# Optimization experiments

Hardware: AMD Instinct MI355X
Metric: run time of the kernel (lower is better)

Reference implementation:

```python
import jax, jax.numpy as jnp
import numpy as np

HEADS = 16
LORA_ALPHA = 1.0
LORA_R = 8.0


def setup_inputs() -> dict:
    key = jax.random.key(0)
    ks = jax.random.split(key, 7)
    B, S, D, R = 4, 2048, 1024, 8
    s = 0.02
    return {
        "x": jax.random.normal(ks[0], (B, S, D), dtype=jnp.float32),
        "lora_A": jax.random.normal(ks[1], (R, D), dtype=jnp.float32) * s,
        "lora_B": jax.random.normal(ks[2], (3 * D, R), dtype=jnp.float32) * s,
        "W_qkv": jax.random.normal(ks[3], (3 * D, D), dtype=jnp.float32) * s,
        "b_qkv": jax.random.normal(ks[4], (3 * D,), dtype=jnp.float32) * s,
        "W_proj": jax.random.normal(ks[5], (D, D), dtype=jnp.float32) * s,
        "b_proj": jax.random.normal(ks[6], (D,), dtype=jnp.float32) * s,
    }


def reference(x, lora_A, lora_B, W_qkv, b_qkv, W_proj, b_proj):
    B, S, D = x.shape
    H = HEADS
    Hd = D // H
    scale = Hd ** -0.5

    # qkv projection: x @ W_qkv.T + b  -> [B, S, 3D]
    qkv = jnp.einsum("bsd,ed->bse", x, W_qkv) + b_qkv
    # LoRA branch: (x @ A.T) @ B.T * (alpha / r)
    lora = jnp.einsum("bsr,er->bse", jnp.einsum("bsd,rd->bsr", x, lora_A), lora_B)
    qkv = qkv + lora * (LORA_ALPHA / LORA_R)

    qkv = qkv.reshape(B, S, 3, H, Hd).transpose(2, 0, 3, 1, 4)
    q, k, v = qkv[0], qkv[1], qkv[2]

    attn = jnp.einsum("bhqd,bhkd->bhqk", q, k) * scale
    attn = jax.nn.softmax(attn, axis=-1)  # dropout is identity in eval mode
    out = jnp.einsum("bhqk,bhkd->bhqd", attn, v)
    out = out.transpose(0, 2, 1, 3).reshape(B, S, D)
    out = jnp.einsum("bsd,ed->bse", out, W_proj) + b_proj
    return out
```

## Files before the change

### kernel.cpp

```cpp
#include <hip/hip_runtime.h>
#include <hip/hip_bf16.h>

typedef __bf16 bf16_t;
typedef __bf16 bf16x8 __attribute__((ext_vector_type(8)));
typedef float f32x4 __attribute__((ext_vector_type(4)));

#define MFMA16(a, b, c) __builtin_amdgcn_mfma_f32_16x16x32_bf16((a), (b), (c), 0, 0, 0)

__device__ __forceinline__ void gload16(const bf16_t* g, bf16_t* l) {
  __builtin_amdgcn_global_load_lds((const __attribute__((address_space(1))) void*)g,
                                   (__attribute__((address_space(3))) void*)l,
                                   16, 0, 0);
}

__global__ void __launch_bounds__(256)
prep_kernel(const float* __restrict__ x, const float* __restrict__ lA,
            const float* __restrict__ lB, const float* __restrict__ Wq,
            const float* __restrict__ Wp,
            bf16_t* __restrict__ xh, bf16_t* __restrict__ We,
            bf16_t* __restrict__ Wph) {
  const int bid = blockIdx.x, tid = threadIdx.x;
  if (bid < 4096) {
    const size_t i = ((size_t)bid * 256 + tid) * 8;
    const float4 f0 = ((const float4*)(x + i))[0];
    const float4 f1 = ((const float4*)(x + i))[1];
    alignas(16) bf16_t o[8] = {(bf16_t)f0.x, (bf16_t)f0.y, (bf16_t)f0.z, (bf16_t)f0.w,
                               (bf16_t)f1.x, (bf16_t)f1.y, (bf16_t)f1.z, (bf16_t)f1.w};
    *(uint4*)(xh + i) = *(const uint4*)o;
  } else if (bid < 7168) {
    const int g = (bid - 4096) * 256 + tid;
    const int e = g >> 8;
    const int d4 = (g & 255) * 4;
    float4 a = ((const float4*)(Wq + (size_t)e * 1024 + d4))[0];
#pragma unroll
    for (int r8 = 0; r8 < 8; ++r8) {
      const float sc = 0.125f * lB[e * 8 + r8];
      const float4 av = ((const float4*)(lA + r8 * 1024 + d4))[0];
      a.x += sc * av.x; a.y += sc * av.y; a.z += sc * av.z; a.w += sc * av.w;
    }
    alignas(8) bf16_t o[4] = {(bf16_t)a.x, (bf16_t)a.y, (bf16_t)a.z, (bf16_t)a.w};
    *(uint2*)(We + (size_t)e * 1024 + d4) = *(const uint2*)o;
  } else {
    const size_t i = ((size_t)(bid - 7168) * 256 + tid) * 8;
    const float4 f0 = ((const float4*)(Wp + i))[0];
    const float4 f1 = ((const float4*)(Wp + i))[1];
    alignas(16) bf16_t o[8] = {(bf16_t)f0.x, (bf16_t)f0.y, (bf16_t)f0.z, (bf16_t)f0.w,
                               (bf16_t)f1.x, (bf16_t)f1.y, (bf16_t)f1.z, (bf16_t)f1.w};
    *(uint4*)(Wph + i) = *(const uint4*)o;
  }
}

template <int EPI>
__global__ void __launch_bounds__(256)
gemm128(const bf16_t* __restrict__ A, const bf16_t* __restrict__ Bw,
        const float* __restrict__ bias, bf16_t* __restrict__ Qb,
        bf16_t* __restrict__ Kb, bf16_t* __restrict__ Vt,
        float* __restrict__ Obuf) {
  __shared__ bf16_t Asm[2][128 * 32];
  __shared__ bf16_t Bsm[2][128 * 32];
  const int tid = threadIdx.x;
  const int lane = tid & 63;
  const int wv = tid >> 6;
  const int wm = (wv >> 1) * 64;
  const int wn = (wv & 1) * 64;
  const int tm = blockIdx.x * 128;
  const int tn = blockIdx.y * 128;
  const int K = 1024;
  const int r = lane & 15, g = lane >> 4;

  const int srow = tid >> 2;
  const int scol = (tid & 3) * 8;
  const bf16_t* gA = A + (size_t)(tm + srow) * K + scol;
  const bf16_t* gB = Bw + (size_t)(tn + srow) * K + scol;

  f32x4 acc[4][4] = {};

  auto stage = [&](int kt, int buf) {
    const int k0 = kt * 32;
    bf16_t* la = &Asm[buf][wv * 512];
    bf16_t* lb = &Bsm[buf][wv * 512];
    gload16(gA + k0, la);
    gload16(gA + (size_t)64 * K + k0, la + 2048);
    gload16(gB + k0, lb);
    gload16(gB + (size_t)64 * K + k0, lb + 2048);
  };

  auto compute = [&](int buf) {
    bf16x8 af[4], bff[4];
#pragma unroll
    for (int mt = 0; mt < 4; ++mt)
      af[mt] = *(const bf16x8*)&Asm[buf][(wm + mt * 16 + r) * 32 + g * 8];
#pragma unroll
    for (int nt = 0; nt < 4; ++nt)
      bff[nt] = *(const bf16x8*)&Bsm[buf][(wn + nt * 16 + r) * 32 + g * 8];
#pragma unroll
    for (int mt = 0; mt < 4; ++mt)
#pragma unroll
      for (int nt = 0; nt < 4; ++nt)
        acc[mt][nt] = MFMA16(af[mt], bff[nt], acc[mt][nt]);
  };

  stage(0, 0);
  __syncthreads();
  int buf = 0;
  for (int kt = 0; kt < 31; ++kt) {
    stage(kt + 1, buf ^ 1);
    compute(buf);
    __syncthreads();
    buf ^= 1;
  }
  compute(buf);

  if (EPI == 0) {
    const int which = tn >> 10;
#pragma unroll
    for (int nt = 0; nt < 4; ++nt) {
      const int e = tn + wn + nt * 16 + r;
      const float bv = bias[e];
      const int h = (e >> 6) & 15;
      const int hd = e & 63;
#pragma unroll
      for (int mt = 0; mt < 4; ++mt) {
        const int m0 = tm + wm + mt * 16 + g * 4;
        const int b = m0 >> 11;
        const int s0 = m0 & 2047;
        const size_t bh = (size_t)(b * 16 + h);
        if (which == 2) {
          alignas(8) bf16_t tmp[4];
#pragma unroll
          for (int j = 0; j < 4; ++j) tmp[j] = (bf16_t)(acc[mt][nt][j] + bv);
          *(uint2*)&Vt[(bh * 64 + hd) * 2048 + s0] = *(const uint2*)tmp;
        } else {
          bf16_t* dst = (which == 0) ? Qb : Kb;
#pragma unroll
          for (int j = 0; j < 4; ++j)
            dst[(bh * 2048 + s0 + j) * 64 + hd] = (bf16_t)(acc[mt][nt][j] + bv);
        }
      }
    }
  } else {
#pragma unroll
    for (int nt = 0; nt < 4; ++nt) {
      const int e = tn + wn + nt * 16 + r;
      const float bv = bias[e];
#pragma unroll
      for (int mt = 0; mt < 4; ++mt) {
#pragma unroll
        for (int j = 0; j < 4; ++j) {
          const int m = tm + wm + mt * 16 + g * 4 + j;
          Obuf[(size_t)m * 1024 + e] = acc[mt][nt][j] + bv;
        }
      }
    }
  }
}

__global__ void __launch_bounds__(256)
attn_kernel(const bf16_t* __restrict__ Qb, const bf16_t* __restrict__ Kb,
            const bf16_t* __restrict__ Vt, bf16_t* __restrict__ AO) {
  __shared__ bf16_t Ks[2][64 * 64];
  __shared__ bf16_t Vs[2][64 * 64];
  __shared__ bf16_t Ps[4][32 * 72];

  const int tid = threadIdx.x, lane = tid & 63, wv = tid >> 6;
  const int bh = blockIdx.x;
  const int qt = blockIdx.y;
  const int r = lane & 15, g = lane >> 4;

  const size_t qrow0 = (size_t)bh * 2048 + qt * 128 + wv * 32;
  bf16x8 qf[2][2];
#pragma unroll
  for (int mt2 = 0; mt2 < 2; ++mt2)
#pragma unroll
    for (int kc = 0; kc < 2; ++kc)
      qf[mt2][kc] = *(const bf16x8*)&Qb[(qrow0 + mt2 * 16 + r) * 64 + kc * 32 + g * 8];

  const int krow = tid >> 3;
  const int kcg = ((tid & 7) ^ (krow & 7)) * 8;
  const bf16_t* gK = Kb + (size_t)bh * 2048 * 64;
  const bf16_t* gV = Vt + (size_t)bh * 64 * 2048;

  auto stageKV = [&](int t, int buf) {
    const int kv0 = t * 64;
    gload16(gK + (size_t)(kv0 + krow) * 64 + kcg, &Ks[buf][wv * 512]);
    gload16(gK + (size_t)(kv0 + 32 + krow) * 64 + kcg, &Ks[buf][2048 + wv * 512]);
    gload16(gV + (size_t)krow * 2048 + kv0 + kcg, &Vs[buf][wv * 512]);
    gload16(gV + (size_t)(32 + krow) * 2048 + kv0 + kcg, &Vs[buf][2048 + wv * 512]);
  };

  f32x4 oacc[2][4] = {};
  float lsum[2][4] = {};

  stageKV(0, 0);
  __syncthreads();
  int buf = 0;
  for (int t = 0; t < 32; ++t) {
    if (t < 31) stageKV(t + 1, buf ^ 1);
    f32x4 sacc[2][4] = {};
#pragma unroll
    for (int ntk = 0; ntk < 4; ++ntk) {
      const int row = ntk * 16 + r;
#pragma unroll
      for (int kc = 0; kc < 2; ++kc) {
        const int cg = (kc * 4 + g) ^ (row & 7);
        const bf16x8 kfrag = *(const bf16x8*)&Ks[buf][row * 64 + cg * 8];
#pragma unroll
        for (int mt2 = 0; mt2 < 2; ++mt2)
          sacc[mt2][ntk] = MFMA16(qf[mt2][kc], kfrag, sacc[mt2][ntk]);
      }
    }
#pragma unroll
    for (int mt2 = 0; mt2 < 2; ++mt2)
#pragma unroll
      for (int ntk = 0; ntk < 4; ++ntk)
#pragma unroll
        for (int j = 0; j < 4; ++j) {
          const float p = __expf(sacc[mt2][ntk][j] * 0.125f);
          lsum[mt2][j] += p;
          Ps[wv][(mt2 * 16 + g * 4 + j) * 72 + ntk * 16 + r] = (bf16_t)p;
        }
    asm volatile("s_waitcnt lgkmcnt(0)" ::: "memory");
    __builtin_amdgcn_sched_barrier(0);
#pragma unroll
    for (int kc = 0; kc < 2; ++kc) {
      bf16x8 pf[2];
#pragma unroll
      for (int mt2 = 0; mt2 < 2; ++mt2)
        pf[mt2] = *(const bf16x8*)&Ps[wv][(mt2 * 16 + r) * 72 + kc * 32 + g * 8];
#pragma unroll
      for (int nth = 0; nth < 4; ++nth) {
        const int hrow = nth * 16 + r;
        const int cg = (kc * 4 + g) ^ (hrow & 7);
        const bf16x8 vfrag = *(const bf16x8*)&Vs[buf][hrow * 64 + cg * 8];
#pragma unroll
        for (int mt2 = 0; mt2 < 2; ++mt2)
          oacc[mt2][nth] = MFMA16(pf[mt2], vfrag, oacc[mt2][nth]);
      }
    }
    __syncthreads();
    buf ^= 1;
  }

#pragma unroll
  for (int m = 1; m < 16; m <<= 1)
#pragma unroll
    for (int mt2 = 0; mt2 < 2; ++mt2)
#pragma unroll
      for (int j = 0; j < 4; ++j)
        lsum[mt2][j] += __shfl_xor(lsum[mt2][j], m, 64);

  const int b = bh >> 4, h = bh & 15;
#pragma unroll
  for (int mt2 = 0; mt2 < 2; ++mt2)
#pragma unroll
    for (int j = 0; j < 4; ++j) {
      const float inv = __builtin_amdgcn_rcpf(lsum[mt2][j]);
      const int s = qt * 128 + wv * 32 + mt2 * 16 + g * 4 + j;
#pragma unroll
      for (int nth = 0; nth < 4; ++nth) {
        const int col = h * 64 + nth * 16 + r;
        AO[((size_t)(b * 2048 + s)) * 1024 + col] = (bf16_t)(oacc[mt2][nth][j] * inv);
      }
    }
}

extern "C" void kernel_launch(void* const* d_in, const int* in_sizes, int n_in,
                              void* d_out, int out_size, void* d_ws, size_t ws_size,
                              hipStream_t stream) {
  const float* x = (const float*)d_in[0];
  const float* lA = (const float*)d_in[1];
  const float* lB = (const float*)d_in[2];
  const float* Wq = (const float*)d_in[3];
  const float* bq = (const float*)d_in[4];
  const float* Wp = (const float*)d_in[5];
  const float* bp = (const float*)d_in[6];

  char* ws = (char*)d_ws;
  bf16_t* xh  = (bf16_t*)(ws);
  bf16_t* We  = (bf16_t*)(ws + 16777216);
  bf16_t* Wph = (bf16_t*)(ws + 23068672);
  bf16_t* Qb  = (bf16_t*)(ws + 25165824);
  bf16_t* Kb  = (bf16_t*)(ws + 41943040);
  bf16_t* Vt  = (bf16_t*)(ws + 58720256);
  bf16_t* AO  = (bf16_t*)(ws + 75497472);

  prep_kernel<<<7680, 256, 0, stream>>>(x, lA, lB, Wq, Wp, xh, We, Wph);
  gemm128<0><<<dim3(64, 24), 256, 0, stream>>>(xh, We, bq, Qb, Kb, Vt, nullptr);
  attn_kernel<<<dim3(64, 16), 256, 0, stream>>>(Qb, Kb, Vt, AO);
  gemm128<1><<<dim3(64, 8), 256, 0, stream>>>(AO, Wph, bp, nullptr, nullptr, nullptr,
                                              (float*)d_out);
}
```

Measured before the change: 331.1 us.

## Load K/V fragments directly from global in attention and prefold softmax scale into Q

The attention kernel drops the LDS double-buffered K/V staging and block-wide barriers, reading K and V MFMA fragments straight from global memory (relying on L1/L2 caching). The score MFMA is transposed (K as A operand) so each lane owns a query row, which simplifies the row-sum reduction and P store layout. The softmax scale times log2(e) is folded into Q in the QKV epilogue so the kernel can use a raw v_exp_f32, and s_setprio plus a 4-waves occupancy bound are added. It trades LDS reuse across waves for more global/L2 traffic and removes synchronization.

After: 427.4 us. 1.29x slower.

```diff
diff --git a/kernel.cpp b/kernel.cpp
--- a/kernel.cpp
+++ b/kernel.cpp
@@ -11,6 +11,12 @@
   __builtin_amdgcn_global_load_lds((const __attribute__((address_space(1))) void*)g,
                                    (__attribute__((address_space(3))) void*)l,
                                    16, 0, 0);
+}
+
+__device__ __forceinline__ float fexp2(float x) {
+  float r;
+  asm("v_exp_f32 %0, %1" : "=v"(r) : "v"(x));
+  return r;
 }
 
 __global__ void __launch_bounds__(256)
@@ -113,6 +119,7 @@
 
   if (EPI == 0) {
     const int which = tn >> 10;
+    const float qs = (which == 0) ? 0.18033688011f : 1.0f;
 #pragma unroll
     for (int nt = 0; nt < 4; ++nt) {
       const int e = tn + wn + nt * 16 + r;
@@ -134,7 +141,7 @@
           bf16_t* dst = (which == 0) ? Qb : Kb;
 #pragma unroll
           for (int j = 0; j < 4; ++j)
-            dst[(bh * 2048 + s0 + j) * 64 + hd] = (bf16_t)(acc[mt][nt][j] + bv);
+            dst[(bh * 2048 + s0 + j) * 64 + hd] = (bf16_t)((acc[mt][nt][j] + bv) * qs);
         }
       }
     }
@@ -155,11 +162,9 @@
   }
 }
 
-__global__ void __launch_bounds__(256)
+__global__ void __launch_bounds__(256, 4)
 attn_kernel(const bf16_t* __restrict__ Qb, const bf16_t* __restrict__ Kb,
             const bf16_t* __restrict__ Vt, bf16_t* __restrict__ AO) {
-  __shared__ bf16_t Ks[2][64 * 64];
-  __shared__ bf16_t Vs[2][64 * 64];
   __shared__ bf16_t Ps[4][32 * 72];
 
   const int tid = threadIdx.x, lane = tid & 63, wv = tid >> 6;
@@ -175,86 +180,73 @@
     for (int kc = 0; kc < 2; ++kc)
       qf[mt2][kc] = *(const bf16x8*)&Qb[(qrow0 + mt2 * 16 + r) * 64 + kc * 32 + g * 8];
 
-  const int krow = tid >> 3;
-  const int kcg = ((tid & 7) ^ (krow & 7)) * 8;
   const bf16_t* gK = Kb + (size_t)bh * 2048 * 64;
   const bf16_t* gV = Vt + (size_t)bh * 64 * 2048;
-
-  auto stageKV = [&](int t, int buf) {
-    const int kv0 = t * 64;
-    gload16(gK + (size_t)(kv0 + krow) * 64 + kcg, &Ks[buf][wv * 512]);
-    gload16(gK + (size_t)(kv0 + 32 + krow) * 64 + kcg, &Ks[buf][2048 + wv * 512]);
-    gload16(gV + (size_t)krow * 2048 + kv0 + kcg, &Vs[buf][wv * 512]);
-    gload16(gV + (size_t)(32 + krow) * 2048 + kv0 + kcg, &Vs[buf][2048 + wv * 512]);
-  };
+  bf16_t* myP = &Ps[wv][0];
 
   f32x4 oacc[2][4] = {};
-  float lsum[2][4] = {};
-
-  stageKV(0, 0);
-  __syncthreads();
-  int buf = 0;
+  float lsum[2] = {0.f, 0.f};
+
   for (int t = 0; t < 32; ++t) {
-    if (t < 31) stageKV(t + 1, buf ^ 1);
+    const int k0 = t * 64;
     f32x4 sacc[2][4] = {};
 #pragma unroll
-    for (int ntk = 0; ntk < 4; ++ntk) {
-      const int row = ntk * 16 + r;
-#pragma unroll
-      for (int kc = 0; kc < 2; ++kc) {
-        const int cg = (kc * 4 + g) ^ (row & 7);
-        const bf16x8 kfrag = *(const bf16x8*)&Ks[buf][row * 64 + cg * 8];
+    for (int kc = 0; kc < 2; ++kc) {
+      bf16x8 kf[4];
+#pragma unroll
+      for (int ntk = 0; ntk < 4; ++ntk)
+        kf[ntk] = *(const bf16x8*)&gK[(size_t)(k0 + ntk * 16 + r) * 64 + kc * 32 + g * 8];
+      __builtin_amdgcn_s_setprio(1);
+#pragma unroll
+      for (int ntk = 0; ntk < 4; ++ntk)
 #pragma unroll
         for (int mt2 = 0; mt2 < 2; ++mt2)
-          sacc[mt2][ntk] = MFMA16(qf[mt2][kc], kfrag, sacc[mt2][ntk]);
-      }
+          sacc[mt2][ntk] = MFMA16(kf[ntk], qf[mt2][kc], sacc[mt2][ntk]);
+      __builtin_amdgcn_s_setprio(0);
     }
 #pragma unroll
     for (int mt2 = 0; mt2 < 2; ++mt2)
 #pragma unroll
-      for (int ntk = 0; ntk < 4; ++ntk)
-#pragma unroll
-        for (int j = 0; j < 4; ++j) {
-          const float p = __expf(sacc[mt2][ntk][j] * 0.125f);
-          lsum[mt2][j] += p;
-          Ps[wv][(mt2 * 16 + g * 4 + j) * 72 + ntk * 16 + r] = (bf16_t)p;
-        }
-    asm volatile("s_waitcnt lgkmcnt(0)" ::: "memory");
-    __builtin_amdgcn_sched_barrier(0);
+      for (int ntk = 0; ntk < 4; ++ntk) {
+        const f32x4 s4 = sacc[mt2][ntk];
+        const float p0 = fexp2(s4[0]), p1 = fexp2(s4[1]);
+        const float p2 = fexp2(s4[2]), p3 = fexp2(s4[3]);
+        lsum[mt2] += (p0 + p1) + (p2 + p3);
+        alignas(8) bf16_t pb[4] = {(bf16_t)p0, (bf16_t)p1, (bf16_t)p2, (bf16_t)p3};
+        *(uint2*)&myP[(mt2 * 16 + r) * 72 + ntk * 16 + g * 4] = *(const uint2*)pb;
+      }
 #pragma unroll
     for (int kc = 0; kc < 2; ++kc) {
-      bf16x8 pf[2];
+      bf16x8 vf[4], pf[2];
+#pragma unroll
+      for (int nth = 0; nth < 4; ++nth)
+        vf[nth] = *(const bf16x8*)&gV[(size_t)(nth * 16 + r) * 2048 + k0 + kc * 32 + g * 8];
 #pragma unroll
       for (int mt2 = 0; mt2 < 2; ++mt2)
-        pf[mt2] = *(const bf16x8*)&Ps[wv][(mt2 * 16 + r) * 72 + kc * 32 + g * 8];
-#pragma unroll
-      for (int nth = 0; nth < 4; ++nth) {
-        const int hrow = nth * 16 + r;
-        const int cg = (kc * 4 + g) ^ (hrow & 7);
-        const bf16x8 vfrag = *(const bf16x8*)&Vs[buf][hrow * 64 + cg * 8];
+        pf[mt2] = *(const bf16x8*)&myP[(mt2 * 16 + r) * 72 + kc * 32 + g * 8];
+      __builtin_amdgcn_s_setprio(1);
+#pragma unroll
+      for (int nth = 0; nth < 4; ++nth)
 #pragma unroll
         for (int mt2 = 0; mt2 < 2; ++mt2)
-          oacc[mt2][nth] = MFMA16(pf[mt2], vfrag, oacc[mt2][nth]);
-      }
-    }
-    __syncthreads();
-    buf ^= 1;
-  }
-
-#pragma unroll
-  for (int m = 1; m < 16; m <<= 1)
-#pragma unroll
-    for (int mt2 = 0; mt2 < 2; ++mt2)
-#pragma unroll
-      for (int j = 0; j < 4; ++j)
-        lsum[mt2][j] += __shfl_xor(lsum[mt2][j], m, 64);
+          oacc[mt2][nth] = MFMA16(pf[mt2], vf[nth], oacc[mt2][nth]);
+      __builtin_amdgcn_s_setprio(0);
+    }
+  }
+
+#pragma unroll
+  for (int mt2 = 0; mt2 < 2; ++mt2) {
+    lsum[mt2] += __shfl_xor(lsum[mt2], 16, 64);
+    lsum[mt2] += __shfl_xor(lsum[mt2], 32, 64);
+  }
 
   const int b = bh >> 4, h = bh & 15;
 #pragma unroll
   for (int mt2 = 0; mt2 < 2; ++mt2)
 #pragma unroll
     for (int j = 0; j < 4; ++j) {
-      const float inv = __builtin_amdgcn_rcpf(lsum[mt2][j]);
+      const float sum = __shfl(lsum[mt2], g * 4 + j, 64);
+      const float inv = __builtin_amdgcn_rcpf(sum);
       const int s = qt * 128 + wv * 32 + mt2 * 16 + g * 4 + j;
 #pragma unroll
       for (int nth = 0; nth < 4; ++nth) {
```
